# Performance work log

Hardware: AMD Instinct MI355X
Metric: run time of the kernel (lower is better)

The kernel has to match this reference:

```python
import jax, jax.numpy as jnp
import numpy as np

B, S, H, L = 64, 512, 768, 9


def setup_inputs() -> dict:
    key = jax.random.key(0)
    ks = jax.random.split(key, 8)
    hidden = jax.random.normal(ks[0], (B, S, H), jnp.float32)
    lengths = jax.random.randint(ks[1], (B,), S // 2, S + 1)
    attention_mask = (jnp.arange(S)[None, :] < lengths[:, None]).astype(jnp.int32)
    labels = jax.random.randint(ks[2], (B, S), 0, L)
    # sprinkle some -100 ignore labels like HF datasets do
    ignore = jax.random.uniform(ks[3], (B, S)) < 0.05
    labels = jnp.where(ignore, -100, labels)
    W = jax.random.normal(ks[4], (H, L), jnp.float32) * 0.02
    b = jnp.zeros((L,), jnp.float32)
    start_transitions = jax.random.uniform(ks[5], (L,), jnp.float32, -0.1, 0.1)
    end_transitions = jax.random.uniform(ks[6], (L,), jnp.float32, -0.1, 0.1)
    transitions = jax.random.uniform(ks[7], (L, L), jnp.float32, -0.1, 0.1)
    return dict(hidden=hidden, attention_mask=attention_mask, labels=labels, W=W, b=b,
                start_transitions=start_transitions, end_transitions=end_transitions,
                transitions=transitions)


def _crf_numerator(emissions, tags, maskf, start_t, end_t, trans):
    # score of the gold tag sequence (torchcrf _compute_score)
    first = start_t[tags[:, 0]] + jnp.take_along_axis(emissions[:, 0], tags[:, 0:1], axis=1)[:, 0]
    em = jnp.take_along_axis(emissions, tags[..., None], axis=2)[..., 0]      # [B,S]
    tr = trans[tags[:, :-1], tags[:, 1:]]                                     # [B,S-1]
    score = first + jnp.sum((em[:, 1:] + tr) * maskf[:, 1:], axis=1)
    last_idx = (jnp.sum(maskf, axis=1).astype(jnp.int32) - 1)
    last_tags = jnp.take_along_axis(tags, last_idx[:, None], axis=1)[:, 0]
    return score + end_t[last_tags]


def _crf_lognorm(emissions, maskf, start_t, end_t, trans):
    # forward algorithm (torchcrf _compute_normalizer) as a lax.scan
    score0 = start_t[None, :] + emissions[:, 0]                               # [B,L]
    em_seq = jnp.transpose(emissions[:, 1:], (1, 0, 2))                       # [S-1,B,L]
    m_seq = maskf[:, 1:].T                                                    # [S-1,B]

    def step(score, xs):
        em_t, m_t = xs
        nxt = jax.nn.logsumexp(score[:, :, None] + trans[None] + em_t[:, None, :], axis=1)
        return jnp.where(m_t[:, None] > 0, nxt, score), None

    score, _ = jax.lax.scan(step, score0, (em_seq, m_seq))
    return jax.nn.logsumexp(score + end_t[None, :], axis=1)


def _viterbi(emissions, maskf, start_t, end_t, trans):
    score0 = start_t[None, :] + emissions[:, 0]                               # [B,L]
    em_seq = jnp.transpose(emissions[:, 1:], (1, 0, 2))
    m_seq = maskf[:, 1:].T

    def step(score, xs):
        em_t, m_t = xs
        cand = score[:, :, None] + trans[None]                                # [B,L,L]
        bp = jnp.argmax(cand, axis=1)                                         # [B,L]
        nxt = jnp.max(cand, axis=1) + em_t
        return jnp.where(m_t[:, None] > 0, nxt, score), bp

    score, history = jax.lax.scan(step, score0, (em_seq, m_seq))              # history [S-1,B,L]
    best_last = jnp.argmax(score + end_t[None, :], axis=1)                    # [B]

    def back(cur, xs):
        bp_t, m_t = xs
        prev = jnp.where(m_t > 0, jnp.take_along_axis(bp_t, cur[:, None], axis=1)[:, 0], cur)
        return prev, prev

    _, tags_rev = jax.lax.scan(back, best_last, (history[::-1], m_seq[::-1]))
    tags = jnp.concatenate([tags_rev[::-1].T, best_last[:, None]], axis=1)    # [B,S]
    return tags


def reference(hidden, attention_mask, labels, W, b, start_transitions, end_transitions, transitions):
    maskf = attention_mask.astype(hidden.dtype)                               # [B,S]
    logits = jnp.einsum('bsh,hl->bsl', hidden, W) + b                         # [B,S,L]
    safe_labels = jnp.where(labels == -100, 0, labels)
    num = _crf_numerator(logits, safe_labels, maskf, start_transitions, end_transitions, transitions)
    den = _crf_lognorm(logits, maskf, start_transitions, end_transitions, transitions)
    loss = -jnp.mean(num - den)                                               # -crf(..., reduction='mean')
    tags = _viterbi(logits, maskf, start_transitions, end_transitions, transitions)
    fake_logits = jax.nn.one_hot(tags, L, dtype=logits.dtype) * maskf[..., None]
    return loss, fake_logits
```

## Files before the change

kernel.cpp:

```cpp
#include <hip/hip_runtime.h>
#include <hip/hip_bf16.h>
#include <stdint.h>

constexpr int BB  = 64;
constexpr int SS  = 512;
constexpr int HH  = 768;
constexpr int NL  = 9;
constexpr int NROWS = BB * SS;
constexpr int EMN   = SS * NL;
constexpr int NSEG  = 8;
constexpr float NEG  = -1e30f;

__device__ __forceinline__ float readlane_f(float v, int lane) {
  union { float f; int i; } u;
  u.f = v;
  u.i = __builtin_amdgcn_readlane(u.i, lane);
  return u.f;
}

__global__ __launch_bounds__(256) void logits_kernel(
    const float* __restrict__ hidden, const float* __restrict__ W,
    const float* __restrict__ bias, const int* __restrict__ mask,
    float* __restrict__ logits, int* __restrict__ lens) {
  __shared__ float wt[NL * HH];
  __shared__ float part[4][64][10];
  const int tid  = threadIdx.x;
  const int lane = tid & 63;
  const int seg  = tid >> 6;

  if (blockIdx.x < 64 && tid < 64) {
    const int4* mp = (const int4*)(mask + blockIdx.x * SS);
    const int4 a = mp[tid];
    const int4 c = mp[tid + 64];
    int lsum = a.x + a.y + a.z + a.w + c.x + c.y + c.z + c.w;
#pragma unroll
    for (int off = 32; off >= 1; off >>= 1) lsum += __shfl_xor(lsum, off, 64);
    if (tid == 0) lens[blockIdx.x] = lsum;
  }

  for (int idx = tid; idx < HH * NL; idx += 256) {
    const int k = idx / NL, l = idx - k * NL;
    wt[l * HH + k] = W[idx];
  }
  __syncthreads();

  const int row = blockIdx.x * 64 + lane;
  const float4* hp = (const float4*)(hidden + (size_t)row * HH + seg * 192);
  const float* wsegbase = wt + seg * 192;
  float acc[NL];
#pragma unroll
  for (int l = 0; l < NL; ++l) acc[l] = 0.0f;

#pragma unroll 4
  for (int kb = 0; kb < 48; ++kb) {
    const float4 h4 = hp[kb];
#pragma unroll
    for (int l = 0; l < NL; ++l) {
      const float4 w4 = *(const float4*)(wsegbase + l * HH + kb * 4);
      acc[l] += h4.x * w4.x + h4.y * w4.y + h4.z * w4.z + h4.w * w4.w;
    }
  }
#pragma unroll
  for (int l = 0; l < NL; ++l) part[seg][lane][l] = acc[l];
  __syncthreads();

  for (int idx = tid; idx < 64 * NL; idx += 256) {
    const int r = idx / NL, l = idx - r * NL;
    logits[(size_t)(blockIdx.x * 64 + r) * NL + l] =
        ((part[0][r][l] + part[1][r][l]) + (part[2][r][l] + part[3][r][l])) +
        bias[l];
  }
}

__global__ __launch_bounds__(64) void scan_kernel(
    const float* __restrict__ logits, const int* __restrict__ labels,
    const float* __restrict__ start_t, const float* __restrict__ end_t,
    const float* __restrict__ trans, float* __restrict__ out,
    float* __restrict__ num_den, const int* __restrict__ lens,
    float* __restrict__ segmat) {
  __shared__ unsigned char bp_s[EMN + 80];
  __shared__ unsigned char tags_s[SS];
  __shared__ int lab[SS];

  const int blk = blockIdx.x;
  const int tid = threadIdx.x;
  const int j   = (tid < NL) ? tid : NL - 1;

  if (blk < 64) {
    const int b   = blk;
    const int len = lens[b];
    const float* emb = logits + (size_t)b * EMN;
    float tc[NL];
#pragma unroll
    for (int i = 0; i < NL; ++i) tc[i] = trans[i * NL + j];
    float s[NL];
#pragma unroll
    for (int i = 0; i < NL; ++i) s[i] = start_t[i] + emb[i];
    float eA = emb[1 * NL + j], eB = emb[2 * NL + j];
    float eC = emb[3 * NL + j], eD = emb[4 * NL + j];
    for (int t = 1; t < len; ++t) {
      float c[NL];
#pragma unroll
      for (int i = 0; i < NL; ++i) c[i] = s[i] + tc[i];
      const float x01 = fmaxf(c[0], c[1]), x23 = fmaxf(c[2], c[3]);
      const float x45 = fmaxf(c[4], c[5]), x67 = fmaxf(c[6], c[7]);
      const float best = fmaxf(fmaxf(fmaxf(x01, x23), fmaxf(x45, x67)), c[8]);
      const float nxt = best + eA;
      {
        const bool b01 = c[0] >= c[1], b23 = c[2] >= c[3];
        const bool b45 = c[4] >= c[5], b67 = c[6] >= c[7];
        const float v01 = b01 ? c[0] : c[1]; const int i01 = b01 ? 0 : 1;
        const float v23 = b23 ? c[2] : c[3]; const int i23 = b23 ? 2 : 3;
        const float v45 = b45 ? c[4] : c[5]; const int i45 = b45 ? 4 : 5;
        const float v67 = b67 ? c[6] : c[7]; const int i67 = b67 ? 6 : 7;
        const bool bA = v01 >= v23, bB = v45 >= v67;
        const float vA = bA ? v01 : v23; const int iA = bA ? i01 : i23;
        const float vB = bB ? v45 : v67; const int iB = bB ? i45 : i67;
        const bool bC = vA >= vB;
        const float vC = bC ? vA : vB; const int iC = bC ? iA : iB;
        const bool bD = vC >= c[8];
        const int arg = bD ? iC : 8;
        bp_s[t * NL + tid] = (unsigned char)arg;
      }
#pragma unroll
      for (int i = 0; i < NL; ++i) s[i] = readlane_f(nxt, i);
      eA = eB; eB = eC; eC = eD;
      eD = emb[(t + 4) * NL + j];
    }
    float bv = s[0] + end_t[0];
    int   bl = 0;
#pragma unroll
    for (int i = 1; i < NL; ++i) {
      const float cc = s[i] + end_t[i];
      if (cc > bv) { bv = cc; bl = i; }
    }
    __syncthreads();

    uint64_t C = 0x876543210ULL;
#pragma unroll
    for (int k = 1; k <= 8; ++k) {
      const int t = 8 * tid + k;
      uint64_t nc = 0;
#pragma unroll
      for (int x = 0; x < 9; ++x) {
        const int g = bp_s[t * NL + x] & 15;
        nc |= ((C >> (4 * g)) & 15ULL) << (4 * x);
      }
      C = (t < len) ? nc : C;
    }
    const uint32_t Clo = (uint32_t)C, Chi = (uint32_t)(C >> 32);
    uint32_t cur = (uint32_t)bl;
    int bnd = 0;
#pragma unroll
    for (int c = 63; c >= 0; --c) {
      bnd = (tid == c) ? (int)cur : bnd;
      const uint32_t lo = (uint32_t)__builtin_amdgcn_readlane((int)Clo, c);
      const uint32_t hi = (uint32_t)__builtin_amdgcn_readlane((int)Chi, c);
      const uint64_t cc = ((uint64_t)hi << 32) | lo;
      cur = (uint32_t)((cc >> (4 * cur)) & 15u);
    }
    int tag = bnd;
#pragma unroll
    for (int k = 8; k >= 1; --k) {
      const int t = 8 * tid + k;
      const int tt = (t < 512) ? t : 511;
      const int nt = bp_s[tt * NL + tag];
      tag = (t < len) ? nt : tag;
      tags_s[t - 1] = (unsigned char)tag;
    }
    __syncthreads();
    for (int i = tid; i < EMN; i += 64) {
      const int t = i / NL;
      const int l = i - t * NL;
      out[1 + (size_t)b * EMN + i] =
          (t < len && l == (int)tags_s[t]) ? 1.0f : 0.0f;
    }

  } else if (blk < 128) {
    const int b   = blk - 64;
    const int len = lens[b];
    const float* emb = logits + (size_t)b * EMN;
    for (int t = tid; t < SS; t += 64) {
      const int v = labels[b * SS + t];
      lab[t] = (v == -100) ? 0 : v;
    }
    __syncthreads();
    float contrib = 0.0f;
    for (int t = tid; t < SS; t += 64) {
      if (t >= 1 && t < len)
        contrib += emb[t * NL + lab[t]] + trans[lab[t - 1] * NL + lab[t]];
    }
#pragma unroll
    for (int off = 32; off >= 1; off >>= 1)
      contrib += __shfl_xor(contrib, off, 64);
    if (tid == 0) {
      const int l0 = lab[0];
      num_den[b] = start_t[l0] + emb[l0] + contrib + end_t[lab[len - 1]];
    }

  } else {
    const int id   = blk - 128;
    const int pair = id / 3;
    const int wv   = id - pair * 3;
    const int b    = pair >> 3;
    const int sg   = pair & 7;
    const int e0   = 3 * wv;
    const int len  = lens[b];
    const float* emb = logits + (size_t)b * EMN;
    float tc[NL];
#pragma unroll
    for (int i = 0; i < NL; ++i) tc[i] = trans[i * NL + j];
    float s0[NL], s1[NL], s2[NL];
#pragma unroll
    for (int i = 0; i < NL; ++i) {
      s0[i] = (i == e0)     ? 0.0f : NEG;
      s1[i] = (i == e0 + 1) ? 0.0f : NEG;
      s2[i] = (i == e0 + 2) ? 0.0f : NEG;
    }
    float my0 = (j == e0)     ? 0.0f : NEG;
    float my1 = (j == e0 + 1) ? 0.0f : NEG;
    float my2 = (j == e0 + 2) ? 0.0f : NEG;
    const int tbeg  = 64 * sg + 1;
    const int tlast = (64 * sg + 64 < 511) ? 64 * sg + 64 : 511;
    float eA = emb[tbeg * NL + j],       eB = emb[(tbeg + 1) * NL + j];
    float eC = emb[(tbeg + 2) * NL + j], eD = emb[(tbeg + 3) * NL + j];
    for (int t = tbeg; t <= tlast; ++t) {
      if (t >= len) break;
      float c0[NL], c1[NL], c2[NL];
#pragma unroll
      for (int i = 0; i < NL; ++i) {
        c0[i] = s0[i] + tc[i];
        c1[i] = s1[i] + tc[i];
        c2[i] = s2[i] + tc[i];
      }
      const float m0 = fmaxf(fmaxf(fmaxf(fmaxf(c0[0], c0[1]), fmaxf(c0[2], c0[3])),
                                   fmaxf(fmaxf(c0[4], c0[5]), fmaxf(c0[6], c0[7]))), c0[8]);
      const float m1 = fmaxf(fmaxf(fmaxf(fmaxf(c1[0], c1[1]), fmaxf(c1[2], c1[3])),
                                   fmaxf(fmaxf(c1[4], c1[5]), fmaxf(c1[6], c1[7]))), c1[8]);
      const float m2 = fmaxf(fmaxf(fmaxf(fmaxf(c2[0], c2[1]), fmaxf(c2[2], c2[3])),
                                   fmaxf(fmaxf(c2[4], c2[5]), fmaxf(c2[6], c2[7]))), c2[8]);
      float u0 = 0.0f, u1 = 0.0f, u2 = 0.0f;
#pragma unroll
      for (int i = 0; i < NL; ++i) {
        u0 += __expf(c0[i] - m0);
        u1 += __expf(c1[i] - m1);
        u2 += __expf(c2[i] - m2);
      }
      my0 = m0 + __logf(u0) + eA;
      my1 = m1 + __logf(u1) + eA;
      my2 = m2 + __logf(u2) + eA;
#pragma unroll
      for (int i = 0; i < NL; ++i) {
        s0[i] = readlane_f(my0, i);
        s1[i] = readlane_f(my1, i);
        s2[i] = readlane_f(my2, i);
      }
      eA = eB; eB = eC; eC = eD;
      eD = emb[(t + 4) * NL + j];
    }
    if (tid < NL) {
      float* M = segmat + (size_t)(b * NSEG + sg) * 81;
      M[(e0    ) * NL + tid] = my0;
      M[(e0 + 1) * NL + tid] = my1;
      M[(e0 + 2) * NL + tid] = my2;
    }
  }
}

__global__ __launch_bounds__(64) void combine_kernel(
    const float* __restrict__ logits, const float* __restrict__ segmat,
    const float* __restrict__ start_t, const float* __restrict__ end_t,
    const float* __restrict__ num_den, float* __restrict__ out) {
  const int b   = blockIdx.x;
  const int tid = threadIdx.x;
  const int j   = (tid < NL) ? tid : NL - 1;
  float s[NL];
#pragma unroll
  for (int i = 0; i < NL; ++i) s[i] = start_t[i] + logits[(size_t)b * EMN + i];
  float mcur[NL], mnxt[NL];
  {
    const float* M = segmat + (size_t)(b * NSEG) * 81;
#pragma unroll
    for (int i = 0; i < NL; ++i) mcur[i] = M[i * NL + j];
  }
  for (int sg = 0; sg < NSEG; ++sg) {
    if (sg + 1 < NSEG) {
      const float* M = segmat + (size_t)(b * NSEG + sg + 1) * 81;
#pragma unroll
      for (int i = 0; i < NL; ++i) mnxt[i] = M[i * NL + j];
    }
    float c[NL];
#pragma unroll
    for (int i = 0; i < NL; ++i) c[i] = s[i] + mcur[i];
    const float x01 = fmaxf(c[0], c[1]), x23 = fmaxf(c[2], c[3]);
    const float x45 = fmaxf(c[4], c[5]), x67 = fmaxf(c[6], c[7]);
    const float m = fmaxf(fmaxf(fmaxf(x01, x23), fmaxf(x45, x67)), c[8]);
    float sum = 0.0f;
#pragma unroll
    for (int i = 0; i < NL; ++i) sum += __expf(c[i] - m);
    const float nxt = m + __logf(sum);
#pragma unroll
    for (int i = 0; i < NL; ++i) s[i] = readlane_f(nxt, i);
#pragma unroll
    for (int i = 0; i < NL; ++i) mcur[i] = mnxt[i];
  }
  float c[NL];
#pragma unroll
  for (int i = 0; i < NL; ++i) c[i] = s[i] + end_t[i];
  const float x01 = fmaxf(c[0], c[1]), x23 = fmaxf(c[2], c[3]);
  const float x45 = fmaxf(c[4], c[5]), x67 = fmaxf(c[6], c[7]);
  const float m = fmaxf(fmaxf(fmaxf(x01, x23), fmaxf(x45, x67)), c[8]);
  float sum = 0.0f;
#pragma unroll
  for (int i = 0; i < NL; ++i) sum += __expf(c[i] - m);
  if (tid == 0) {
    const float den = m + __logf(sum);
    atomicAdd(out, (den - num_den[b]) * (1.0f / 64.0f));
  }
}

extern "C" void kernel_launch(void* const* d_in, const int* in_sizes, int n_in,
                              void* d_out, int out_size, void* d_ws, size_t ws_size,
                              hipStream_t stream) {
  const float* hidden  = (const float*)d_in[0];
  const int*   mask    = (const int*)d_in[1];
  const int*   labels  = (const int*)d_in[2];
  const float* W       = (const float*)d_in[3];
  const float* bias    = (const float*)d_in[4];
  const float* start_t = (const float*)d_in[5];
  const float* end_t   = (const float*)d_in[6];
  const float* trans   = (const float*)d_in[7];
  float* out = (float*)d_out;

  float* logits  = (float*)d_ws;
  float* segmat  = logits + (size_t)NROWS * NL;
  float* num_den = segmat + (size_t)BB * NSEG * 81;
  int*   lens    = (int*)(num_den + 128);

  hipMemsetAsync(out, 0, sizeof(float), stream);
  logits_kernel<<<512, 256, 0, stream>>>(hidden, W, bias, mask, logits, lens);
  scan_kernel<<<1664, 64, 0, stream>>>(logits, labels, start_t, end_t, trans,
                                       out, num_den, lens, segmat);
  combine_kernel<<<64, 64, 0, stream>>>(logits, segmat, start_t, end_t,
                                        num_den, out);
}
```

Before: 264.1 us.

## Stage hidden rows through swizzled LDS tiles with coalesced loads; unroll Viterbi recurrence

The logits GEMV no longer has each lane stream its own row with strided float4 loads. Each wave now loads 8 rows by 32 floats per chunk with coalesced accesses, double-buffered in registers, writes them to an XOR-swizzled shared tile, and reads them back per lane. The Viterbi scan is unrolled by 8 with an 8-deep emission prefetch ring and raises wave priority with s_setprio. The cost is extra LDS traffic and more registers in exchange for better global-memory coalescing and fewer loop overheads on the serial scan.

Measured after the change: 291.7 us. +10.5%, slower.

```diff
diff --git a/kernel.cpp b/kernel.cpp
--- a/kernel.cpp
+++ b/kernel.cpp
@@ -22,11 +22,12 @@
     const float* __restrict__ hidden, const float* __restrict__ W,
     const float* __restrict__ bias, const int* __restrict__ mask,
     float* __restrict__ logits, int* __restrict__ lens) {
-  __shared__ float wt[NL * HH];
+  __shared__ __align__(16) float wt[NL * HH];
+  __shared__ __align__(16) float tiles[4][64 * 32];
   __shared__ float part[4][64][10];
   const int tid  = threadIdx.x;
   const int lane = tid & 63;
-  const int seg  = tid >> 6;
+  const int kq   = tid >> 6;
 
   if (blockIdx.x < 64 && tid < 64) {
     const int4* mp = (const int4*)(mask + blockIdx.x * SS);
@@ -44,29 +45,47 @@
   }
   __syncthreads();
 
-  const int row = blockIdx.x * 64 + lane;
-  const float4* hp = (const float4*)(hidden + (size_t)row * HH + seg * 192);
-  const float* wsegbase = wt + seg * 192;
+  const int rowbase = blockIdx.x * 64;
+  const int r8  = lane >> 3;
+  const int c4  = lane & 7;
+  const int c4s = c4 ^ r8;
+  const float4* hsrc = (const float4*)hidden +
+                       (size_t)(rowbase + r8) * 192 + kq * 48 + c4;
+  float4* tile4 = (float4*)tiles[kq];
   float acc[NL];
 #pragma unroll
   for (int l = 0; l < NL; ++l) acc[l] = 0.0f;
 
-#pragma unroll 4
-  for (int kb = 0; kb < 48; ++kb) {
-    const float4 h4 = hp[kb];
-#pragma unroll
-    for (int l = 0; l < NL; ++l) {
-      const float4 w4 = *(const float4*)(wsegbase + l * HH + kb * 4);
-      acc[l] += h4.x * w4.x + h4.y * w4.y + h4.z * w4.z + h4.w * w4.w;
-    }
-  }
-#pragma unroll
-  for (int l = 0; l < NL; ++l) part[seg][lane][l] = acc[l];
+  float4 rbuf[8];
+#pragma unroll
+  for (int i = 0; i < 8; ++i) rbuf[i] = hsrc[(size_t)i * 8 * 192];
+  for (int ch = 0; ch < 6; ++ch) {
+#pragma unroll
+    for (int i = 0; i < 8; ++i) tile4[(r8 + 8 * i) * 8 + c4s] = rbuf[i];
+    if (ch < 5) {
+#pragma unroll
+      for (int i = 0; i < 8; ++i)
+        rbuf[i] = hsrc[(size_t)i * 8 * 192 + (ch + 1) * 8];
+    }
+#pragma unroll
+    for (int g = 0; g < 8; ++g) {
+      const float4 h4 = tile4[lane * 8 + (g ^ (lane & 7))];
+      const int k = kq * 192 + ch * 32 + g * 4;
+      const float* wb = wt + k;
+#pragma unroll
+      for (int l = 0; l < NL; ++l) {
+        const float4 w4 = *(const float4*)(wb + l * HH);
+        acc[l] += h4.x * w4.x + h4.y * w4.y + h4.z * w4.z + h4.w * w4.w;
+      }
+    }
+  }
+#pragma unroll
+  for (int l = 0; l < NL; ++l) part[kq][lane][l] = acc[l];
   __syncthreads();
 
   for (int idx = tid; idx < 64 * NL; idx += 256) {
     const int r = idx / NL, l = idx - r * NL;
-    logits[(size_t)(blockIdx.x * 64 + r) * NL + l] =
+    logits[(size_t)(rowbase + r) * NL + l] =
         ((part[0][r][l] + part[1][r][l]) + (part[2][r][l] + part[3][r][l])) +
         bias[l];
   }
@@ -87,6 +106,7 @@
   const int j   = (tid < NL) ? tid : NL - 1;
 
   if (blk < 64) {
+    asm volatile("s_setprio 3");
     const int b   = blk;
     const int len = lens[b];
     const float* emb = logits + (size_t)b * EMN;
@@ -96,16 +116,50 @@
     float s[NL];
 #pragma unroll
     for (int i = 0; i < NL; ++i) s[i] = start_t[i] + emb[i];
-    float eA = emb[1 * NL + j], eB = emb[2 * NL + j];
-    float eC = emb[3 * NL + j], eD = emb[4 * NL + j];
-    for (int t = 1; t < len; ++t) {
+    float e[8];
+#pragma unroll
+    for (int i = 0; i < 8; ++i) e[i] = emb[(1 + i) * NL + j];
+    int t = 1;
+    for (; t + 8 <= len; t += 8) {
+#pragma unroll
+      for (int u = 0; u < 8; ++u) {
+        const int tt = t + u;
+        float c[NL];
+#pragma unroll
+        for (int i = 0; i < NL; ++i) c[i] = s[i] + tc[i];
+        const float x01 = fmaxf(c[0], c[1]), x23 = fmaxf(c[2], c[3]);
+        const float x45 = fmaxf(c[4], c[5]), x67 = fmaxf(c[6], c[7]);
+        const float best = fmaxf(fmaxf(fmaxf(x01, x23), fmaxf(x45, x67)), c[8]);
+        const float nxt = best + e[u];
+        {
+          const bool b01 = c[0] >= c[1], b23 = c[2] >= c[3];
+          const bool b45 = c[4] >= c[5], b67 = c[6] >= c[7];
+          const float v01 = b01 ? c[0] : c[1]; const int i01 = b01 ? 0 : 1;
+          const float v23 = b23 ? c[2] : c[3]; const int i23 = b23 ? 2 : 3;
+          const float v45 = b45 ? c[4] : c[5]; const int i45 = b45 ? 4 : 5;
+          const float v67 = b67 ? c[6] : c[7]; const int i67 = b67 ? 6 : 7;
+          const bool bA = v01 >= v23, bB = v45 >= v67;
+          const float vA = bA ? v01 : v23; const int iA = bA ? i01 : i23;
+          const float vB = bB ? v45 : v67; const int iB = bB ? i45 : i67;
+          const bool bC = vA >= vB;
+          const float vC = bC ? vA : vB; const int iC = bC ? iA : iB;
+          const bool bD = vC >= c[8];
+          const int arg = bD ? iC : 8;
+          bp_s[tt * NL + tid] = (unsigned char)arg;
+        }
+        e[u] = emb[(tt + 8) * NL + j];
+#pragma unroll
+        for (int i = 0; i < NL; ++i) s[i] = readlane_f(nxt, i);
+      }
+    }
+    for (int u = 0; t < len; ++t, ++u) {
       float c[NL];
 #pragma unroll
       for (int i = 0; i < NL; ++i) c[i] = s[i] + tc[i];
       const float x01 = fmaxf(c[0], c[1]), x23 = fmaxf(c[2], c[3]);
       const float x45 = fmaxf(c[4], c[5]), x67 = fmaxf(c[6], c[7]);
       const float best = fmaxf(fmaxf(fmaxf(x01, x23), fmaxf(x45, x67)), c[8]);
-      const float nxt = best + eA;
+      const float nxt = best + e[u];
       {
         const bool b01 = c[0] >= c[1], b23 = c[2] >= c[3];
         const bool b45 = c[4] >= c[5], b67 = c[6] >= c[7];
@@ -124,8 +178,6 @@
       }
 #pragma unroll
       for (int i = 0; i < NL; ++i) s[i] = readlane_f(nxt, i);
-      eA = eB; eB = eC; eC = eD;
-      eD = emb[(t + 4) * NL + j];
     }
     float bv = s[0] + end_t[0];
     int   bl = 0;
@@ -139,14 +191,14 @@
     uint64_t C = 0x876543210ULL;
 #pragma unroll
     for (int k = 1; k <= 8; ++k) {
-      const int t = 8 * tid + k;
+      const int tk = 8 * tid + k;
       uint64_t nc = 0;
 #pragma unroll
       for (int x = 0; x < 9; ++x) {
-        const int g = bp_s[t * NL + x] & 15;
+        const int g = bp_s[tk * NL + x] & 15;
         nc |= ((C >> (4 * g)) & 15ULL) << (4 * x);
       }
-      C = (t < len) ? nc : C;
+      C = (tk < len) ? nc : C;
     }
     const uint32_t Clo = (uint32_t)C, Chi = (uint32_t)(C >> 32);
     uint32_t cur = (uint32_t)bl;
@@ -162,18 +214,18 @@
     int tag = bnd;
 #pragma unroll
     for (int k = 8; k >= 1; --k) {
-      const int t = 8 * tid + k;
-      const int tt = (t < 512) ? t : 511;
-      const int nt = bp_s[tt * NL + tag];
-      tag = (t < len) ? nt : tag;
-      tags_s[t - 1] = (unsigned char)tag;
+      const int tk = 8 * tid + k;
+      const int tkk = (tk < 512) ? tk : 511;
+      const int nt = bp_s[tkk * NL + tag];
+      tag = (tk < len) ? nt : tag;
+      tags_s[tk - 1] = (unsigned char)tag;
     }
     __syncthreads();
     for (int i = tid; i < EMN; i += 64) {
-      const int t = i / NL;
-      const int l = i - t * NL;
+      const int tt = i / NL;
+      const int l = i - tt * NL;
       out[1 + (size_t)b * EMN + i] =
-          (t < len && l == (int)tags_s[t]) ? 1.0f : 0.0f;
+          (tt < len && l == (int)tags_s[tt]) ? 1.0f : 0.0f;
     }
 
   } else if (blk < 128) {
```
